# Performance work log

Hardware: AMD Instinct MI355X
Metric: run time of the kernel (lower is better)

## Reference

```python
import jax, jax.numpy as jnp
import numpy as np

THRESH = 1.0
DECAY = 0.5


def setup_inputs() -> dict:
    key = jax.random.key(0)
    X = jax.random.normal(key, (32, 128, 32, 32, 16), dtype=jnp.float32)
    return {"X": X}


def reference(X):
    # Leaky-integrate-and-fire scan over the trailing time axis.
    Xt = jnp.moveaxis(X, -1, 0)  # [T, B, C, H, W] time-leading for scan

    def step(mem, x_t):
        mem = mem * DECAY + x_t                      # leaky integration
        s = (mem >= THRESH).astype(X.dtype)          # threshold spike
        mem = mem * (1.0 - s)                        # hard reset on spike
        return mem, s

    _, spikes = jax.lax.scan(step, jnp.zeros_like(Xt[0]), Xt)
    return jnp.moveaxis(spikes, 0, -1)  # back to [..., T]
```

## Files before the change

kernel.cpp:

```cpp
#include <hip/hip_runtime.h>


#define LIF_DECAY  0.5f
#define LIF_THRESH 1.0f

__global__ __launch_bounds__(256) void lif_kernel(const float* __restrict__ X,
                                                  float* __restrict__ out,
                                                  int n_pixels) {
    int p = blockIdx.x * blockDim.x + threadIdx.x;
    if (p >= n_pixels) return;

    const float4* __restrict__ xin = reinterpret_cast<const float4*>(X) + (size_t)p * 4;
    float4* __restrict__ oout      = reinterpret_cast<float4*>(out) + (size_t)p * 4;

    float4 v0 = xin[0];
    float4 v1 = xin[1];
    float4 v2 = xin[2];
    float4 v3 = xin[3];

    float x[16] = {v0.x, v0.y, v0.z, v0.w,
                   v1.x, v1.y, v1.z, v1.w,
                   v2.x, v2.y, v2.z, v2.w,
                   v3.x, v3.y, v3.z, v3.w};
    float s[16];

    float mem = 0.0f;
#pragma unroll
    for (int t = 0; t < 16; ++t) {
        mem = mem * LIF_DECAY + x[t];
        float spike = (mem >= LIF_THRESH) ? 1.0f : 0.0f;
        s[t] = spike;
        mem = (spike != 0.0f) ? 0.0f : mem;
    }

    oout[0] = make_float4(s[0],  s[1],  s[2],  s[3]);
    oout[1] = make_float4(s[4],  s[5],  s[6],  s[7]);
    oout[2] = make_float4(s[8],  s[9],  s[10], s[11]);
    oout[3] = make_float4(s[12], s[13], s[14], s[15]);
}

extern "C" void kernel_launch(void* const* d_in, const int* in_sizes, int n_in,
                              void* d_out, int out_size, void* d_ws, size_t ws_size,
                              hipStream_t stream) {
    (void)n_in; (void)d_ws; (void)ws_size; (void)out_size;
    const float* X = (const float*)d_in[0];
    float* out = (float*)d_out;

    const int T = 16;
    int n_pixels = in_sizes[0] / T;

    const int block = 256;
    int grid = (n_pixels + block - 1) / block;
    lif_kernel<<<grid, block, 0, stream>>>(X, out, n_pixels);
}
```

Baseline: 437.0 us.

## Stage loads and stores through LDS for fully coalesced float4 access

```diff
diff --git a/kernel.cpp b/kernel.cpp
--- a/kernel.cpp
+++ b/kernel.cpp
@@ -4,52 +4,64 @@
 #define LIF_DECAY  0.5f
 #define LIF_THRESH 1.0f
 
-__global__ __launch_bounds__(256) void lif_kernel(const float* __restrict__ X,
-                                                  float* __restrict__ out,
-                                                  int n_pixels) {
-    int p = blockIdx.x * blockDim.x + threadIdx.x;
-    if (p >= n_pixels) return;
-
-    const float4* __restrict__ xin = reinterpret_cast<const float4*>(X) + (size_t)p * 4;
-    float4* __restrict__ oout      = reinterpret_cast<float4*>(out) + (size_t)p * 4;
-
-    float4 v0 = xin[0];
-    float4 v1 = xin[1];
-    float4 v2 = xin[2];
-    float4 v3 = xin[3];
-
-    float x[16] = {v0.x, v0.y, v0.z, v0.w,
-                   v1.x, v1.y, v1.z, v1.w,
-                   v2.x, v2.y, v2.z, v2.w,
-                   v3.x, v3.y, v3.z, v3.w};
-    float s[16];
-
-    float mem = 0.0f;
-#pragma unroll
-    for (int t = 0; t < 16; ++t) {
-        mem = mem * LIF_DECAY + x[t];
-        float spike = (mem >= LIF_THRESH) ? 1.0f : 0.0f;
-        s[t] = spike;
-        mem = (spike != 0.0f) ? 0.0f : mem;
+#define LIF_STEP(v)                                        \
+    {                                                      \
+        m = m * LIF_DECAY + (v);                           \
+        float sp = (m >= LIF_THRESH) ? 1.0f : 0.0f;        \
+        (v) = sp;                                          \
+        m = (sp != 0.0f) ? 0.0f : m;                       \
     }
 
-    oout[0] = make_float4(s[0],  s[1],  s[2],  s[3]);
-    oout[1] = make_float4(s[4],  s[5],  s[6],  s[7]);
-    oout[2] = make_float4(s[8],  s[9],  s[10], s[11]);
-    oout[3] = make_float4(s[12], s[13], s[14], s[15]);
+__global__ __launch_bounds__(256) void lif_kernel(const float4* __restrict__ X4,
+                                                  float4* __restrict__ O4) {
+    __shared__ float4 lds[4 * 257];
+
+    const int tid = threadIdx.x;
+    const size_t base = (size_t)blockIdx.x * 1024;
+
+    const int q  = tid & 3;
+    const int plc = (tid >> 2);
+
+#pragma unroll
+    for (int k = 0; k < 4; ++k) {
+        float4 v = X4[base + (size_t)(k * 256 + tid)];
+        lds[q * 257 + (k * 64 + plc)] = v;
+    }
+    __syncthreads();
+
+    float4 f0 = lds[0 * 257 + tid];
+    float4 f1 = lds[1 * 257 + tid];
+    float4 f2 = lds[2 * 257 + tid];
+    float4 f3 = lds[3 * 257 + tid];
+
+    float m = 0.0f;
+    LIF_STEP(f0.x) LIF_STEP(f0.y) LIF_STEP(f0.z) LIF_STEP(f0.w)
+    LIF_STEP(f1.x) LIF_STEP(f1.y) LIF_STEP(f1.z) LIF_STEP(f1.w)
+    LIF_STEP(f2.x) LIF_STEP(f2.y) LIF_STEP(f2.z) LIF_STEP(f2.w)
+    LIF_STEP(f3.x) LIF_STEP(f3.y) LIF_STEP(f3.z) LIF_STEP(f3.w)
+
+    __syncthreads();
+
+    lds[0 * 257 + tid] = f0;
+    lds[1 * 257 + tid] = f1;
+    lds[2 * 257 + tid] = f2;
+    lds[3 * 257 + tid] = f3;
+    __syncthreads();
+
+#pragma unroll
+    for (int k = 0; k < 4; ++k) {
+        O4[base + (size_t)(k * 256 + tid)] = lds[q * 257 + (k * 64 + plc)];
+    }
 }
 
 extern "C" void kernel_launch(void* const* d_in, const int* in_sizes, int n_in,
                               void* d_out, int out_size, void* d_ws, size_t ws_size,
                               hipStream_t stream) {
     (void)n_in; (void)d_ws; (void)ws_size; (void)out_size;
-    const float* X = (const float*)d_in[0];
-    float* out = (float*)d_out;
+    const float4* X4 = (const float4*)d_in[0];
+    float4* O4 = (float4*)d_out;
 
-    const int T = 16;
-    int n_pixels = in_sizes[0] / T;
-
-    const int block = 256;
-    int grid = (n_pixels + block - 1) / block;
-    lif_kernel<<<grid, block, 0, stream>>>(X, out, n_pixels);
+    int n_f4 = in_sizes[0] / 4;
+    int grid = n_f4 / 1024;
+    lif_kernel<<<grid, 256, 0, stream>>>(X4, O4);
 }
```

New measurement: 427.7 us. -2.1%, faster.
